# Kernel optimization log

Measured on AMD Instinct MI355X. Metric: run time of the kernel, lower is better.

Reference implementation:

```python
import jax, jax.numpy as jnp
import numpy as np

B, T, C = 2, 2048, 2048
H, HKV = 32, 8
D = C // H            # head_dim = 64
G = H // HKV          # groups = 4
ROPE_BASE = 10000.0


def _rotate_half(x):
    x1, x2 = jnp.split(x, 2, axis=-1)
    return jnp.concatenate((-x2, x1), axis=-1)


def _rope_tables(seq_len, dim):
    inv_freq = 1.0 / (ROPE_BASE ** (jnp.arange(0, dim, 2, dtype=jnp.float32) / dim))
    t = jnp.arange(seq_len, dtype=jnp.float32)
    freqs = jnp.outer(t, inv_freq)          # [T, D/2]
    emb = jnp.concatenate((freqs, freqs), axis=-1)  # [T, D]
    return jnp.cos(emb), jnp.sin(emb)


def setup_inputs() -> dict:
    key = jax.random.key(0)
    ks = jax.random.split(key, 5)
    s = 0.02
    return {
        "x": jax.random.normal(ks[0], (B, T, C), jnp.float32),
        "Wq": jax.random.normal(ks[1], (C, C), jnp.float32) * s,
        "Wk": jax.random.normal(ks[2], (HKV * D, C), jnp.float32) * s,
        "Wv": jax.random.normal(ks[3], (HKV * D, C), jnp.float32) * s,
        "Wo": jax.random.normal(ks[4], (C, C), jnp.float32) * s,
    }


def reference(x, Wq, Wk, Wv, Wo):
    b, t, c = x.shape
    # fused QKV projections (nn.Linear: y = x @ W.T)
    q = (x @ Wq.T).reshape(b, t, H, D).transpose(0, 2, 1, 3)      # [B,H,T,D]
    k = (x @ Wk.T).reshape(b, t, HKV, D).transpose(0, 2, 1, 3)    # [B,HKV,T,D]
    v = (x @ Wv.T).reshape(b, t, HKV, D).transpose(0, 2, 1, 3)

    # RoPE (start_pos = 0)
    cos, sin = _rope_tables(t, D)           # [T, D] each
    cos = cos[None, None]                   # [1,1,T,D]
    sin = sin[None, None]
    q = q * cos + _rotate_half(q) * sin
    k = k * cos + _rotate_half(k) * sin

    # GQA head expansion (repeat_interleave on head dim)
    k = jnp.repeat(k, G, axis=1)            # [B,H,T,D]
    v = jnp.repeat(v, G, axis=1)

    # causal attention
    scale = 1.0 / jnp.sqrt(jnp.asarray(D, jnp.float32))
    scores = jnp.einsum('bhqd,bhkd->bhqk', q, k) * scale          # [B,H,T,T]
    causal = jnp.tril(jnp.ones((t, t), dtype=bool))
    scores = jnp.where(causal[None, None], scores, -jnp.inf)
    attn = jax.nn.softmax(scores.astype(jnp.float32), axis=-1).astype(q.dtype)
    out = jnp.einsum('bhqk,bhkd->bhqd', attn, v)                  # [B,H,T,D]
    out = out.transpose(0, 2, 1, 3).reshape(b, t, c)
    return out @ Wo.T
```

## Files before the change

### kernel.cpp

```cpp
#include <hip/hip_runtime.h>
#include <hip/hip_bf16.h>
#include <math.h>

typedef short short8 __attribute__((ext_vector_type(8)));
typedef float floatx4 __attribute__((ext_vector_type(4)));
typedef unsigned int uintx4 __attribute__((ext_vector_type(4)));
typedef int intx2 __attribute__((ext_vector_type(2)));

typedef __attribute__((address_space(1))) unsigned int as1_u32;
typedef __attribute__((address_space(3))) unsigned int as3_u32;

__device__ __forceinline__ void load_lds16(const void* g, void* l) {
  __builtin_amdgcn_global_load_lds((const as1_u32*)g, (as3_u32*)l, 16, 0, 0);
}

__device__ __forceinline__ unsigned short f2bf(float f) {
  __bf16 h = (__bf16)f;
  return __builtin_bit_cast(unsigned short, h);
}

__device__ __forceinline__ unsigned int pack_bf16(float a, float b) {
  return (unsigned int)f2bf(a) | ((unsigned int)f2bf(b) << 16);
}

#define MFMA16(a, b, c) __builtin_amdgcn_mfma_f32_16x16x32_bf16(a, b, c, 0, 0, 0)

#define TB 2
#define TT 2048
#define TC 2048
#define QKN 2560
#define KOFF 2048
#define SCALE_Q 0.18033688f

__global__ __launch_bounds__(256) void cast_all(
    const float* __restrict__ x, const float* __restrict__ wq,
    const float* __restrict__ wk, const float* __restrict__ wv,
    const float* __restrict__ wo,
    unsigned short* __restrict__ xb, unsigned short* __restrict__ wqkv,
    unsigned short* __restrict__ wob, float2* __restrict__ ropeTab) {
  if (blockIdx.x < 256) {
    const int idx = blockIdx.x * 256 + threadIdx.x;
    const int t = idx >> 5, d = idx & 31;
    const float inv = exp2f((float)d * -0.4152410119f);
    float sn, cs;
    sincosf((float)t * inv, &sn, &cs);
    ropeTab[idx] = make_float2(cs, sn);
  }
  long i4 = (long)blockIdx.x * 256 + threadIdx.x;
  const float* src;
  unsigned short* dst;
  if (i4 < 2097152)      { src = x;  dst = xb; }
  else if (i4 < 3145728) { src = wq; dst = wqkv;           i4 -= 2097152; }
  else if (i4 < 3407872) { src = wk; dst = wqkv + 4194304; i4 -= 3145728; }
  else if (i4 < 3670016) { src = wv; dst = wqkv + 5242880; i4 -= 3407872; }
  else                   { src = wo; dst = wob;            i4 -= 3670016; }
  float4 v = ((const float4*)src)[i4];
  ushort4 o;
  o.x = f2bf(v.x); o.y = f2bf(v.y); o.z = f2bf(v.z); o.w = f2bf(v.w);
  ((ushort4*)dst)[i4] = o;
}

#define QKV_MFMA(BF)                                                           \
  __builtin_amdgcn_s_setprio(1);                                               \
  _Pragma("unroll") for (int i_ = 0; i_ < 4; ++i_) {                           \
    _Pragma("unroll") for (int j_ = 0; j_ < 3; ++j_) {                         \
      acc[i_][JBASE + j_] = MFMA16(af[i_][0], BF[j_][0], acc[i_][JBASE + j_]); \
      acc[i_][JBASE + j_] = MFMA16(af[i_][1], BF[j_][1], acc[i_][JBASE + j_]); \
    }                                                                          \
  }                                                                            \
  __builtin_amdgcn_s_setprio(0);

__global__ __launch_bounds__(512, 2) void gemm_qkv(const unsigned short* __restrict__ A,
                                                   const unsigned short* __restrict__ Bw,
                                                   unsigned short* __restrict__ qk,
                                                   unsigned short* __restrict__ vT,
                                                   const float2* __restrict__ ropeTab) {
  extern __shared__ char dynlds[];
  const int K = 2048;
  const int tid = threadIdx.x;
  const int lane = tid & 63, w = tid >> 6;
  const int quad = lane >> 4, l15 = lane & 15;
  const int wm = w >> 1, wn = w & 1;

  const int lin = blockIdx.y * 16 + blockIdx.x;
  const int wg = (lin & 7) * 32 + (lin >> 3);
  const int m0 = (wg >> 4) * 256;
  const int n0 = (wg & 15) * 192;

  floatx4 acc[4][6];
#pragma unroll
  for (int i = 0; i < 4; ++i)
#pragma unroll
    for (int j = 0; j < 6; ++j) acc[i][j] = (floatx4){0.f, 0.f, 0.f, 0.f};

  const int srow8 = tid >> 3;
  const int schk = (tid & 7) ^ (srow8 & 7);
  const unsigned short* aS = A + (size_t)(m0 + srow8) * K + schk * 8;
  const unsigned short* bS = Bw + (size_t)(n0 + srow8) * K + schk * 8;

  const int key0 = (quad ^ (l15 & 7)) << 4;
  const int key1 = ((4 + quad) ^ (l15 & 7)) << 4;
  const int rdA = (wm * 64 + l15) * 128;
  const int rdBl = 32768 + l15 * 128;

  constexpr int F0[6] = {0, 2, 1, 3, 4, 6};
  constexpr int F1[6] = {5, 7, 8, 10, 9, 11};

  auto stageA = [&](int bb, int tt) {
    char* d = dynlds + bb * 57344;
    const unsigned short* s = aS + (size_t)tt * 64;
    load_lds16(s, d + tid * 16);
    load_lds16(s + (size_t)64 * K, d + 8192 + tid * 16);
    load_lds16(s + (size_t)128 * K, d + 16384 + tid * 16);
    load_lds16(s + (size_t)192 * K, d + 24576 + tid * 16);
  };
  auto stageB = [&](int bb, int tt) {
    char* d = dynlds + bb * 57344 + 32768;
    const unsigned short* s = bS + (size_t)tt * 64;
    load_lds16(s, d + tid * 16);
    load_lds16(s + (size_t)64 * K, d + 8192 + tid * 16);
    load_lds16(s + (size_t)128 * K, d + 16384 + tid * 16);
  };

  stageA(0, 0); stageB(0, 0); stageA(1, 1);
  asm volatile("s_waitcnt vmcnt(4)" ::: "memory");
  __builtin_amdgcn_s_barrier();

  short8 af[4][2], bfL[3][2], bfR[3][2];
  const char* cb0 = dynlds;
  const char* cb1 = dynlds + 57344;
  const int NIT = K >> 7;

  for (int it = 0; it < NIT; ++it) {
    const int tO = it * 2 + 1, tE2 = it * 2 + 2, tO2 = it * 2 + 3;
    const bool STG = (it < NIT - 1);

#pragma unroll
    for (int i = 0; i < 4; ++i) {
      af[i][0] = *(const short8*)(cb0 + rdA + i * 2048 + key0);
      af[i][1] = *(const short8*)(cb0 + rdA + i * 2048 + key1);
    }
#pragma unroll
    for (int j = 0; j < 3; ++j) {
      const int fe = wn ? F1[j] : F0[j];
      bfL[j][0] = *(const short8*)(cb0 + rdBl + fe * 2048 + key0);
      bfL[j][1] = *(const short8*)(cb0 + rdBl + fe * 2048 + key1);
    }
    stageB(1, tO);
    __builtin_amdgcn_s_barrier();
    asm volatile("s_waitcnt lgkmcnt(0)" ::: "memory");
    {
      const int JBASE = 0;
      QKV_MFMA(bfL)
    }
    __builtin_amdgcn_s_barrier();

#pragma unroll
    for (int j = 0; j < 3; ++j) {
      const int fe = wn ? F1[3 + j] : F0[3 + j];
      bfR[j][0] = *(const short8*)(cb0 + rdBl + fe * 2048 + key0);
      bfR[j][1] = *(const short8*)(cb0 + rdBl + fe * 2048 + key1);
    }
    if (STG) {
      stageA(0, tE2);
      asm volatile("s_waitcnt vmcnt(4)" ::: "memory");
    } else {
      asm volatile("s_waitcnt vmcnt(0)" ::: "memory");
    }
    __builtin_amdgcn_s_barrier();
    asm volatile("s_waitcnt lgkmcnt(0)" ::: "memory");
    {
      const int JBASE = 3;
      QKV_MFMA(bfR)
    }
    __builtin_amdgcn_s_barrier();

#pragma unroll
    for (int i = 0; i < 4; ++i) {
      af[i][0] = *(const short8*)(cb1 + rdA + i * 2048 + key0);
      af[i][1] = *(const short8*)(cb1 + rdA + i * 2048 + key1);
    }
#pragma unroll
    for (int j = 0; j < 3; ++j) {
      const int fe = wn ? F1[j] : F0[j];
      bfL[j][0] = *(const short8*)(cb1 + rdBl + fe * 2048 + key0);
      bfL[j][1] = *(const short8*)(cb1 + rdBl + fe * 2048 + key1);
    }
    if (STG) stageB(0, tE2);
    __builtin_amdgcn_s_barrier();
    asm volatile("s_waitcnt lgkmcnt(0)" ::: "memory");
    {
      const int JBASE = 0;
      QKV_MFMA(bfL)
    }
    __builtin_amdgcn_s_barrier();

#pragma unroll
    for (int j = 0; j < 3; ++j) {
      const int fe = wn ? F1[3 + j] : F0[3 + j];
      bfR[j][0] = *(const short8*)(cb1 + rdBl + fe * 2048 + key0);
      bfR[j][1] = *(const short8*)(cb1 + rdBl + fe * 2048 + key1);
    }
    if (STG) {
      stageA(1, tO2);
      asm volatile("s_waitcnt vmcnt(4)" ::: "memory");
    } else {
      asm volatile("s_waitcnt vmcnt(0)" ::: "memory");
    }
    __builtin_amdgcn_s_barrier();
    asm volatile("s_waitcnt lgkmcnt(0)" ::: "memory");
    {
      const int JBASE = 3;
      QKV_MFMA(bfR)
    }
    __builtin_amdgcn_s_barrier();
  }

#pragma unroll
  for (int i = 0; i < 4; ++i) {
    const int rowb = m0 + wm * 64 + i * 16 + quad * 4;
    const int tb = rowb & (TT - 1);
#pragma unroll
    for (int jp = 0; jp < 6; jp += 2) {
      const int fe = wn ? F1[jp] : F0[jp];
      const int col = n0 + fe * 16 + l15;
      if (col < QKN) {
        const float qscale = (col < KOFF) ? SCALE_Q : 1.0f;
        const int d = (fe & 3) * 16 + l15;
#pragma unroll
        for (int r = 0; r < 4; ++r) {
          const float2 cssn = ropeTab[(tb + r) * 32 + d];
          const float a = acc[i][jp][r], b2 = acc[i][jp + 1][r];
          const float qa = (a * cssn.x - b2 * cssn.y) * qscale;
          const float qb = (b2 * cssn.x + a * cssn.y) * qscale;
          unsigned short* p = qk + (size_t)(rowb + r) * QKN + col;
          p[0] = f2bf(qa);
          p[32] = f2bf(qb);
        }
      } else {
#pragma unroll
        for (int jj = jp; jj < jp + 2; ++jj) {
          const int fv = wn ? F1[jj] : F0[jj];
          const int colv = n0 + fv * 16 + l15;
          ushort4 pk;
          pk.x = f2bf(acc[i][jj][0]); pk.y = f2bf(acc[i][jj][1]);
          pk.z = f2bf(acc[i][jj][2]); pk.w = f2bf(acc[i][jj][3]);
          *(ushort4*)(vT + (size_t)(colv - 2560) * 4096 + rowb) = pk;
        }
      }
    }
  }
}

#define NT_MFMA(J0, BF)                                                        \
  __builtin_amdgcn_s_setprio(1);                                               \
  _Pragma("unroll") for (int i_ = 0; i_ < 4; ++i_) {                           \
    _Pragma("unroll") for (int j_ = 0; j_ < 2; ++j_) {                         \
      acc[i_][(J0) + j_] = MFMA16(af[i_][0], BF[j_][0], acc[i_][(J0) + j_]);   \
      acc[i_][(J0) + j_] = MFMA16(af[i_][1], BF[j_][1], acc[i_][(J0) + j_]);   \
    }                                                                          \
  }                                                                            \
  __builtin_amdgcn_s_setprio(0);

__global__ __launch_bounds__(512, 2) void gemm_nt_f32(const unsigned short* __restrict__ A,
                                                      const unsigned short* __restrict__ Bw,
                                                      float* __restrict__ C,
                                                      int M, int N, int Kdim) {
  extern __shared__ char dynlds[];
  const int K = 2048;
  const int tid = threadIdx.x;
  const int lane = tid & 63, w = tid >> 6;
  const int quad = lane >> 4, l15 = lane & 15;
  const int wm = w >> 1, wn = w & 1;

  const int lin = blockIdx.y * 16 + blockIdx.x;
  const int wg = (lin & 7) * 32 + (lin >> 3);
  const int m0 = (wg >> 4) * 256;
  const int n0 = (wg & 15) * 128;

  floatx4 acc[4][4];
#pragma unroll
  for (int i = 0; i < 4; ++i)
#pragma unroll
    for (int j = 0; j < 4; ++j) acc[i][j] = (floatx4){0.f, 0.f, 0.f, 0.f};

  const int srow8 = tid >> 3;
  const int schk = (tid & 7) ^ (srow8 & 7);
  const unsigned short* aS = A + (size_t)(m0 + srow8) * K + schk * 8;
  const unsigned short* bS = Bw + (size_t)(n0 + srow8) * K + schk * 8;

  const int key0 = (quad ^ (l15 & 7)) << 4;
  const int key1 = ((4 + quad) ^ (l15 & 7)) << 4;
  const int rdA = (wm * 64 + l15) * 128;
  const int rdB = 32768 + (wn * 64 + l15) * 128;

  auto stage = [&](int bb, int slot, int tt) {
    char* d = dynlds + bb * 49152 + slot * 16384;
    const unsigned short* s =
        (slot == 2 ? bS : aS + (size_t)(slot * 128) * K) + (size_t)tt * 64;
    load_lds16(s, d + tid * 16);
    load_lds16(s + (size_t)64 * K, d + 8192 + tid * 16);
  };

  stage(0, 0, 0); stage(0, 1, 0); stage(0, 2, 0);
  stage(1, 0, 1); stage(1, 1, 1);
  asm volatile("s_waitcnt vmcnt(4)" ::: "memory");
  __builtin_amdgcn_s_barrier();

  short8 af[4][2], bfL[2][2], bfR[2][2];
  const char* cb0 = dynlds;
  const char* cb1 = dynlds + 49152;
  const int NIT = K >> 7;

  for (int it = 0; it < NIT; ++it) {
    const int tO = it * 2 + 1, tE2 = it * 2 + 2, tO2 = it * 2 + 3;
    const bool STG = (it < NIT - 1);

#pragma unroll
    for (int i = 0; i < 4; ++i) {
      af[i][0] = *(const short8*)(cb0 + rdA + i * 2048 + key0);
      af[i][1] = *(const short8*)(cb0 + rdA + i * 2048 + key1);
    }
#pragma unroll
    for (int j = 0; j < 2; ++j) {
      bfL[j][0] = *(const short8*)(cb0 + rdB + j * 2048 + key0);
      bfL[j][1] = *(const short8*)(cb0 + rdB + j * 2048 + key1);
    }
    stage(1, 2, tO);
    __builtin_amdgcn_s_barrier();
    asm volatile("s_waitcnt lgkmcnt(0)" ::: "memory");
    NT_MFMA(0, bfL)
    __builtin_amdgcn_s_barrier();

#pragma unroll
    for (int j = 0; j < 2; ++j) {
      bfR[j][0] = *(const short8*)(cb0 + rdB + (2 + j) * 2048 + key0);
      bfR[j][1] = *(const short8*)(cb0 + rdB + (2 + j) * 2048 + key1);
    }
    if (STG) {
      stage(0, 0, tE2); stage(0, 1, tE2);
      asm volatile("s_waitcnt vmcnt(4)" ::: "memory");
    } else {
      asm volatile("s_waitcnt vmcnt(0)" ::: "memory");
    }
    __builtin_amdgcn_s_barrier();
    asm volatile("s_waitcnt lgkmcnt(0)" ::: "memory");
    NT_MFMA(2, bfR)
    __builtin_amdgcn_s_barrier();

#pragma unroll
    for (int i = 0; i < 4; ++i) {
      af[i][0] = *(const short8*)(cb1 + rdA + i * 2048 + key0);
      af[i][1] = *(const short8*)(cb1 + rdA + i * 2048 + key1);
    }
#pragma unroll
    for (int j = 0; j < 2; ++j) {
      bfL[j][0] = *(const short8*)(cb1 + rdB + j * 2048 + key0);
      bfL[j][1] = *(const short8*)(cb1 + rdB + j * 2048 + key1);
    }
    if (STG) stage(0, 2, tE2);
    __builtin_amdgcn_s_barrier();
    asm volatile("s_waitcnt lgkmcnt(0)" ::: "memory");
    NT_MFMA(0, bfL)
    __builtin_amdgcn_s_barrier();

#pragma unroll
    for (int j = 0; j < 2; ++j) {
      bfR[j][0] = *(const short8*)(cb1 + rdB + (2 + j) * 2048 + key0);
      bfR[j][1] = *(const short8*)(cb1 + rdB + (2 + j) * 2048 + key1);
    }
    if (STG) {
      stage(1, 0, tO2); stage(1, 1, tO2);
      asm volatile("s_waitcnt vmcnt(4)" ::: "memory");
    } else {
      asm volatile("s_waitcnt vmcnt(0)" ::: "memory");
    }
    __builtin_amdgcn_s_barrier();
    asm volatile("s_waitcnt lgkmcnt(0)" ::: "memory");
    NT_MFMA(2, bfR)
    __builtin_amdgcn_s_barrier();
  }

#pragma unroll
  for (int i = 0; i < 4; ++i) {
    const int row = m0 + wm * 64 + i * 16 + quad * 4;
#pragma unroll
    for (int j = 0; j < 4; ++j) {
      const int col = n0 + wn * 64 + j * 16 + l15;
#pragma unroll
      for (int r = 0; r < 4; ++r)
        C[(size_t)(row + r) * N + col] = acc[i][j][r];
    }
  }
}

__global__ __launch_bounds__(256, 3) void attn_kernel(const unsigned short* __restrict__ qk,
                                                      const unsigned short* __restrict__ vT,
                                                      unsigned short* __restrict__ attn) {
  const int h = blockIdx.x, b = blockIdx.y;
  const int qt = 15 - (int)blockIdx.z;
  const int hk = h >> 2;
  const int tid = threadIdx.x;
  const int w = tid >> 6, lane = tid & 63, quad = lane >> 4, l15 = lane & 15;

  __shared__ char lds[32768];

  const int srow = tid >> 3;
  const int sgrp = ((tid & 7) ^ (srow & 7));
  const int relbase = w * 32 + l15;

  const short8 ones = {16256, 16256, 16256, 16256, 16256, 16256, 16256, 16256};

  const size_t rowQ = (size_t)(b * TT + qt * 128);

  {
    const unsigned short* qsrc = qk + (rowQ + srow) * QKN + h * 64 + sgrp * 8;
#pragma unroll
    for (int p = 0; p < 4; ++p)
      load_lds16(qsrc + (size_t)p * 32 * QKN, lds + p * 4096 + tid * 16);
  }
  __syncthreads();
  short8 qf[2][2];
#pragma unroll
  for (int i = 0; i < 2; ++i)
#pragma unroll
    for (int ks = 0; ks < 2; ++ks)
      qf[i][ks] = *(const short8*)(lds + (w * 32 + i * 16 + l15) * 128 +
                                   ((((ks << 2) + quad) ^ (l15 & 7)) << 4));
  __syncthreads();

  floatx4 accO[2][4], accL[2];
#pragma unroll
  for (int i = 0; i < 2; ++i) {
    accL[i] = (floatx4){0.f, 0.f, 0.f, 0.f};
#pragma unroll
    for (int j = 0; j < 4; ++j) accO[i][j] = (floatx4){0.f, 0.f, 0.f, 0.f};
  }

  const unsigned short* kptr =
      qk + (size_t)(b * TT + srow) * QKN + KOFF + hk * 64 + sgrp * 8;
  const unsigned short* vptr =
      vT + (size_t)(hk * 64 + srow) * 4096 + b * TT + sgrp * 8;

  load_lds16(kptr, lds + tid * 16);
  load_lds16(kptr + (size_t)32 * QKN, lds + 4096 + tid * 16);
  load_lds16(vptr, lds + 16384 + tid * 16);
  load_lds16(vptr + (size_t)32 * 4096, lds + 16384 + 4096 + tid * 16);
  kptr += (size_t)64 * QKN;
  vptr += 64;
  __syncthreads();

  auto step = [&](const int BUF, const bool PREF, const int MREL) {
    if (PREF) {
      char* kd = lds + ((BUF ^ 1) * 8192);
      char* vd = lds + 16384 + ((BUF ^ 1) * 8192);
      load_lds16(kptr, kd + tid * 16);
      load_lds16(kptr + (size_t)32 * QKN, kd + 4096 + tid * 16);
      load_lds16(vptr, vd + tid * 16);
      load_lds16(vptr + (size_t)32 * 4096, vd + 4096 + tid * 16);
      kptr += (size_t)64 * QKN;
      vptr += 64;
    }

    const char* Ks = lds + BUF * 8192;
    floatx4 st[2][4];
    __builtin_amdgcn_s_setprio(1);
#pragma unroll
    for (int jm = 0; jm < 4; ++jm) {
      const int krow = jm * 16 + l15;
      const short8 kf0 = *(const short8*)(Ks + krow * 128 + ((quad ^ (l15 & 7)) << 4));
      const short8 kf1 = *(const short8*)(Ks + krow * 128 + (((4 + quad) ^ (l15 & 7)) << 4));
#pragma unroll
      for (int i = 0; i < 2; ++i) {
        floatx4 z = (floatx4){0.f, 0.f, 0.f, 0.f};
        z = __builtin_amdgcn_mfma_f32_16x16x32_bf16(kf0, qf[i][0], z, 0, 0, 0);
        st[i][jm] = __builtin_amdgcn_mfma_f32_16x16x32_bf16(kf1, qf[i][1], z, 0, 0, 0);
      }
    }
    __builtin_amdgcn_s_setprio(0);

    const char* Vt = lds + 16384 + BUF * 8192;
    short8 vf[2][4];
#pragma unroll
    for (int ks = 0; ks < 2; ++ks)
#pragma unroll
      for (int jd = 0; jd < 4; ++jd) {
        const int d = jd * 16 + l15;
        vf[ks][jd] = *(const short8*)(Vt + d * 128 +
                                      ((((ks << 2) + quad) ^ (l15 & 7)) << 4));
      }

    short8 pT[2][2];
#pragma unroll
    for (int i = 0; i < 2; ++i) {
      unsigned int U[4][2];
#pragma unroll
      for (int jm = 0; jm < 4; ++jm) {
        float e0 = __builtin_amdgcn_exp2f(st[i][jm][0]);
        float e1 = __builtin_amdgcn_exp2f(st[i][jm][1]);
        float e2 = __builtin_amdgcn_exp2f(st[i][jm][2]);
        float e3 = __builtin_amdgcn_exp2f(st[i][jm][3]);
        if (MREL >= 0) {
          const int rel = relbase + i * 16 - MREL;
          const int kg = jm * 16 + quad * 4;
          if (kg > rel) e0 = 0.f;
          if (kg + 1 > rel) e1 = 0.f;
          if (kg + 2 > rel) e2 = 0.f;
          if (kg + 3 > rel) e3 = 0.f;
        }
        U[jm][0] = pack_bf16(e0, e1);
        U[jm][1] = pack_bf16(e2, e3);
      }
#pragma unroll
      for (int ks = 0; ks < 2; ++ks) {
        uintx4 t;
#pragma unroll
        for (int hh = 0; hh < 2; ++hh) {
          intx2 r32 = __builtin_amdgcn_permlane32_swap(
              (int)U[2 * ks][hh], (int)U[2 * ks + 1][hh], false, false);
          intx2 r16 = __builtin_amdgcn_permlane16_swap(r32[0], r32[1], false, false);
          t[hh] = (unsigned int)r16[0];
          t[2 + hh] = (unsigned int)r16[1];
        }
        pT[i][ks] = __builtin_bit_cast(short8, t);
      }
    }

    __builtin_amdgcn_s_setprio(1);
#pragma unroll
    for (int ks = 0; ks < 2; ++ks) {
      accL[0] = __builtin_amdgcn_mfma_f32_16x16x32_bf16(pT[0][ks], ones, accL[0], 0, 0, 0);
      accL[1] = __builtin_amdgcn_mfma_f32_16x16x32_bf16(pT[1][ks], ones, accL[1], 0, 0, 0);
#pragma unroll
      for (int jd = 0; jd < 4; ++jd) {
        accO[0][jd] = __builtin_amdgcn_mfma_f32_16x16x32_bf16(pT[0][ks], vf[ks][jd], accO[0][jd], 0, 0, 0);
        accO[1][jd] = __builtin_amdgcn_mfma_f32_16x16x32_bf16(pT[1][ks], vf[ks][jd], accO[1][jd], 0, 0, 0);
      }
    }
    __builtin_amdgcn_s_setprio(0);
    __syncthreads();
  };

  for (int t2 = 0; t2 < qt; ++t2) {
    step(0, true, -1);
    step(1, true, -1);
  }
  step(0, true, 0);
  step(1, false, 64);

#pragma unroll
  for (int i2 = 0; i2 < 2; ++i2) {
    floatx4 rl;
#pragma unroll
    for (int r = 0; r < 4; ++r) rl[r] = __builtin_amdgcn_rcpf(accL[i2][r]);
#pragma unroll
    for (int jd = 0; jd < 4; ++jd) {
      const int col = h * 64 + jd * 16 + l15;
#pragma unroll
      for (int r = 0; r < 4; ++r) {
        const size_t row = rowQ + w * 32 + i2 * 16 + quad * 4 + r;
        attn[row * TC + col] = f2bf(accO[i2][jd][r] * rl[r]);
      }
    }
  }
}

extern "C" void kernel_launch(void* const* d_in, const int* in_sizes, int n_in,
                              void* d_out, int out_size, void* d_ws, size_t ws_size,
                              hipStream_t stream) {
  const float* x = (const float*)d_in[0];
  const float* Wq = (const float*)d_in[1];
  const float* Wk = (const float*)d_in[2];
  const float* Wv = (const float*)d_in[3];
  const float* Wo = (const float*)d_in[4];
  float* out = (float*)d_out;

  char* ws = (char*)d_ws;
  unsigned short* xb   = (unsigned short*)(ws);
  unsigned short* wqkv = (unsigned short*)(ws + 16777216);
  unsigned short* wob  = (unsigned short*)(ws + 29360128);
  unsigned short* qk   = (unsigned short*)(ws + 37748736);
  unsigned short* vT   = (unsigned short*)(ws + 58720256);
  unsigned short* attn = (unsigned short*)(ws + 62914560);
  float2* ropeTab = (float2*)(ws + 62914560);

  cast_all<<<18432, 256, 0, stream>>>(x, Wq, Wk, Wv, Wo, xb, wqkv, wob, ropeTab);
  gemm_qkv<<<dim3(16, 16), 512, 114688, stream>>>(xb, wqkv, qk, vT, ropeTab);
  attn_kernel<<<dim3(32, 2, 16), 256, 0, stream>>>(qk, vT, attn);
  gemm_nt_f32<<<dim3(16, 16), 512, 98304, stream>>>(attn, wob, out, 4096, TC, 2048);
}
```

Measured before the change: 246.4 us.

## Drop mid-stage barriers in GEMM pipelines and raise attention occupancy

In the QKV and output-projection GEMM main loops, the barrier between staging and each MFMA block is removed. The global-load wait (vmcnt) now sits after the MFMA block instead of before it, so global loads overlap with compute and each half-iteration needs one fewer barrier. The attention kernel's launch bounds go from 3 to 4 blocks per CU, which caps registers per thread lower. Removing barriers risks LDS races if a buffer being staged is still being read by other waves, and the tighter register cap may cause spills.

```diff
diff --git a/kernel.cpp b/kernel.cpp
--- a/kernel.cpp
+++ b/kernel.cpp
@@ -147,7 +147,6 @@
       bfL[j][1] = *(const short8*)(cb0 + rdBl + fe * 2048 + key1);
     }
     stageB(1, tO);
-    __builtin_amdgcn_s_barrier();
     asm volatile("s_waitcnt lgkmcnt(0)" ::: "memory");
     {
       const int JBASE = 0;
@@ -161,18 +160,14 @@
       bfR[j][0] = *(const short8*)(cb0 + rdBl + fe * 2048 + key0);
       bfR[j][1] = *(const short8*)(cb0 + rdBl + fe * 2048 + key1);
     }
-    if (STG) {
-      stageA(0, tE2);
-      asm volatile("s_waitcnt vmcnt(4)" ::: "memory");
-    } else {
-      asm volatile("s_waitcnt vmcnt(0)" ::: "memory");
-    }
-    __builtin_amdgcn_s_barrier();
+    if (STG) stageA(0, tE2);
     asm volatile("s_waitcnt lgkmcnt(0)" ::: "memory");
     {
       const int JBASE = 3;
       QKV_MFMA(bfR)
     }
+    if (STG) asm volatile("s_waitcnt vmcnt(4)" ::: "memory");
+    else     asm volatile("s_waitcnt vmcnt(0)" ::: "memory");
     __builtin_amdgcn_s_barrier();
 
 #pragma unroll
@@ -187,7 +182,6 @@
       bfL[j][1] = *(const short8*)(cb1 + rdBl + fe * 2048 + key1);
     }
     if (STG) stageB(0, tE2);
-    __builtin_amdgcn_s_barrier();
     asm volatile("s_waitcnt lgkmcnt(0)" ::: "memory");
     {
       const int JBASE = 0;
@@ -201,18 +195,14 @@
       bfR[j][0] = *(const short8*)(cb1 + rdBl + fe * 2048 + key0);
       bfR[j][1] = *(const short8*)(cb1 + rdBl + fe * 2048 + key1);
     }
-    if (STG) {
-      stageA(1, tO2);
-      asm volatile("s_waitcnt vmcnt(4)" ::: "memory");
-    } else {
-      asm volatile("s_waitcnt vmcnt(0)" ::: "memory");
-    }
-    __builtin_amdgcn_s_barrier();
+    if (STG) stageA(1, tO2);
     asm volatile("s_waitcnt lgkmcnt(0)" ::: "memory");
     {
       const int JBASE = 3;
       QKV_MFMA(bfR)
     }
+    if (STG) asm volatile("s_waitcnt vmcnt(4)" ::: "memory");
+    else     asm volatile("s_waitcnt vmcnt(0)" ::: "memory");
     __builtin_amdgcn_s_barrier();
   }
 
@@ -327,7 +317,6 @@
       bfL[j][1] = *(const short8*)(cb0 + rdB + j * 2048 + key1);
     }
     stage(1, 2, tO);
-    __builtin_amdgcn_s_barrier();
     asm volatile("s_waitcnt lgkmcnt(0)" ::: "memory");
     NT_MFMA(0, bfL)
     __builtin_amdgcn_s_barrier();
@@ -337,15 +326,11 @@
       bfR[j][0] = *(const short8*)(cb0 + rdB + (2 + j) * 2048 + key0);
       bfR[j][1] = *(const short8*)(cb0 + rdB + (2 + j) * 2048 + key1);
     }
-    if (STG) {
-      stage(0, 0, tE2); stage(0, 1, tE2);
-      asm volatile("s_waitcnt vmcnt(4)" ::: "memory");
-    } else {
-      asm volatile("s_waitcnt vmcnt(0)" ::: "memory");
-    }
-    __builtin_amdgcn_s_barrier();
+    if (STG) { stage(0, 0, tE2); stage(0, 1, tE2); }
     asm volatile("s_waitcnt lgkmcnt(0)" ::: "memory");
     NT_MFMA(2, bfR)
+    if (STG) asm volatile("s_waitcnt vmcnt(4)" ::: "memory");
+    else     asm volatile("s_waitcnt vmcnt(0)" ::: "memory");
     __builtin_amdgcn_s_barrier();
 
 #pragma unroll
@@ -359,7 +344,6 @@
       bfL[j][1] = *(const short8*)(cb1 + rdB + j * 2048 + key1);
     }
     if (STG) stage(0, 2, tE2);
-    __builtin_amdgcn_s_barrier();
     asm volatile("s_waitcnt lgkmcnt(0)" ::: "memory");
     NT_MFMA(0, bfL)
     __builtin_amdgcn_s_barrier();
@@ -369,15 +353,11 @@
       bfR[j][0] = *(const short8*)(cb1 + rdB + (2 + j) * 2048 + key0);
       bfR[j][1] = *(const short8*)(cb1 + rdB + (2 + j) * 2048 + key1);
     }
-    if (STG) {
-      stage(1, 0, tO2); stage(1, 1, tO2);
-      asm volatile("s_waitcnt vmcnt(4)" ::: "memory");
-    } else {
-      asm volatile("s_waitcnt vmcnt(0)" ::: "memory");
-    }
-    __builtin_amdgcn_s_barrier();
+    if (STG) { stage(1, 0, tO2); stage(1, 1, tO2); }
     asm volatile("s_waitcnt lgkmcnt(0)" ::: "memory");
     NT_MFMA(2, bfR)
+    if (STG) asm volatile("s_waitcnt vmcnt(4)" ::: "memory");
+    else     asm volatile("s_waitcnt vmcnt(0)" ::: "memory");
     __builtin_amdgcn_s_barrier();
   }
 
@@ -394,7 +374,7 @@
   }
 }
 
-__global__ __launch_bounds__(256, 3) void attn_kernel(const unsigned short* __restrict__ qk,
+__global__ __launch_bounds__(256, 4) void attn_kernel(const unsigned short* __restrict__ qk,
                                                       const unsigned short* __restrict__ vT,
                                                       unsigned short* __restrict__ attn) {
   const int h = blockIdx.x, b = blockIdx.y;
```

Result: slower. 312.6 us (+26.9%).
